# Kernel tuning notes

Measured on AMD Instinct MI355X. Metric: run time of the kernel, lower is better.

## Reference

```python
import jax, jax.numpy as jnp
import numpy as np

B, T, C = 4, 2048, 1024
H = 16
D = C // H  # head_dim = 64


def setup_inputs() -> dict:
    key = jax.random.key(0)
    ks = jax.random.split(key, 9)
    s = 1.0 / np.sqrt(C)
    return {
        "x": jax.random.normal(ks[0], (B, T, C), dtype=jnp.float32),
        "Wq": jax.random.normal(ks[1], (C, C), dtype=jnp.float32) * s,
        "bq": jnp.zeros((C,), dtype=jnp.float32),
        "Wk": jax.random.normal(ks[2], (C, C), dtype=jnp.float32) * s,
        "bk": jnp.zeros((C,), dtype=jnp.float32),
        "Wv": jax.random.normal(ks[3], (C, C), dtype=jnp.float32) * s,
        "bv": jnp.zeros((C,), dtype=jnp.float32),
        "Wp": jax.random.normal(ks[4], (C, C), dtype=jnp.float32) * s,
        "bp": jnp.zeros((C,), dtype=jnp.float32),
    }


def reference(x, Wq, bq, Wk, bk, Wv, bv, Wp, bp):
    # Linear projections; reshape to [B, H, T, D]
    def split_heads(y):
        return y.reshape(B, T, H, D).transpose(0, 2, 1, 3)

    q = split_heads(x @ Wq + bq)
    k = split_heads(x @ Wk + bk)
    v = split_heads(x @ Wv + bv)

    scale = 1.0 / np.sqrt(D)
    att = jnp.einsum('bhqd,bhkd->bhqk', q, k) * scale  # [B,H,T,T]
    att = jax.nn.softmax(att, axis=-1)
    # dropout with p=0.0 is identity
    out = jnp.einsum('bhqk,bhkd->bhqd', att, v)        # [B,H,T,D]
    out = out.transpose(0, 2, 1, 3).reshape(B, T, C)
    return out @ Wp + bp
```

## Files before the change

### kernel.cpp

```cpp
#include <hip/hip_runtime.h>


#define B_ 4
#define T_ 2048
#define C_ 1024
#define H_ 16
#define D_ 64

typedef float  f32x4  __attribute__((ext_vector_type(4)));
typedef __bf16 bf16x8 __attribute__((ext_vector_type(8)));
typedef __bf16 bf16x4 __attribute__((ext_vector_type(4)));
typedef __bf16 bf16x2 __attribute__((ext_vector_type(2)));
typedef unsigned uint2v __attribute__((ext_vector_type(2)));

typedef const __attribute__((address_space(1))) void gv_t;
typedef __attribute__((address_space(3))) void lds_t;

__device__ __forceinline__ void async_load16(const void* g, void* l) {
  __builtin_amdgcn_global_load_lds((gv_t*)g, (lds_t*)l, 16, 0, 0);
}

__device__ __forceinline__ float fast_exp2(float x) {
#if __has_builtin(__builtin_amdgcn_exp2f)
  return __builtin_amdgcn_exp2f(x);
#else
  return exp2f(x);
#endif
}

__device__ __forceinline__ void pl16_swap(unsigned& a, unsigned& b) {
#if __has_builtin(__builtin_amdgcn_permlane16_swap)
  uint2v r = __builtin_amdgcn_permlane16_swap(a, b, false, false);
  a = r[0];
  b = r[1];
#else
  asm("v_permlane16_swap_b32 %0, %1" : "+v"(a), "+v"(b));
#endif
}

__global__ __launch_bounds__(256) void cast_f32_bf16(
    const float* __restrict__ in, __bf16* __restrict__ out, int n) {
  int i = (blockIdx.x * 256 + threadIdx.x) * 8;
  if (i >= n) return;
  float4 a = *(const float4*)(in + i);
  float4 b = *(const float4*)(in + i + 4);
  bf16x8 o;
  o[0] = (__bf16)a.x; o[1] = (__bf16)a.y; o[2] = (__bf16)a.z; o[3] = (__bf16)a.w;
  o[4] = (__bf16)b.x; o[5] = (__bf16)b.y; o[6] = (__bf16)b.z; o[7] = (__bf16)b.w;
  *(bf16x8*)(out + i) = o;
}

__global__ __launch_bounds__(256) void transpose_cast_w(
    const float* __restrict__ W0, const float* __restrict__ W1,
    const float* __restrict__ W2, const float* __restrict__ W3,
    __bf16* __restrict__ out) {
  int z = blockIdx.z;
  const float* W = (z == 0) ? W0 : (z == 1) ? W1 : (z == 2) ? W2 : W3;
  __bf16* o = out + (size_t)z * (C_ * C_);
  __shared__ __align__(16) __bf16 sT[64][72];
  int tid = threadIdx.x;
  int n0 = blockIdx.x * 64, k0 = blockIdx.y * 64;
#pragma unroll
  for (int i = 0; i < 4; i++) {
    int s = tid + i * 256;
    int kr = s >> 4, nc = (s & 15) * 4;
    float4 v = *(const float4*)&W[(size_t)(k0 + kr) * C_ + n0 + nc];
    bf16x4 t;
    t[0] = (__bf16)v.x; t[1] = (__bf16)v.y; t[2] = (__bf16)v.z; t[3] = (__bf16)v.w;
    *(bf16x4*)&sT[kr][nc] = t;
  }
  __syncthreads();
#pragma unroll
  for (int i = 0; i < 2; i++) {
    int s = tid + i * 256;
    int nr = s >> 3, kc = (s & 7) * 8;
    bf16x8 ov;
#pragma unroll
    for (int j = 0; j < 8; j++) ov[j] = sT[kc + j][nr];
    *(bf16x8*)&o[(size_t)(n0 + nr) * C_ + k0 + kc] = ov;
  }
}

template <typename OutT, int EPI>
__device__ __forceinline__ void gemm_body(
    const __bf16* __restrict__ A, const __bf16* __restrict__ Bt,
    const float* __restrict__ bias, OutT* __restrict__ C, int M, int N, int K) {
  __shared__ __align__(16) __bf16 sA[128 * 32];
  __shared__ __align__(16) __bf16 sB[128 * 32];
  int tid = threadIdx.x, lane = tid & 63, wave = tid >> 6;
  int lr = lane & 15, quad = lane >> 4;
  int m0 = blockIdx.y * 128, n0 = blockIdx.x * 128;
  int wm = (wave & 1) * 64, wn = (wave >> 1) * 64;

  const f32x4 zero = {0.f, 0.f, 0.f, 0.f};
  f32x4 acc[4][4];
#pragma unroll
  for (int i = 0; i < 4; i++)
#pragma unroll
    for (int j = 0; j < 4; j++) acc[i][j] = zero;

  for (int k0 = 0; k0 < K; k0 += 32) {
    __syncthreads();
#pragma unroll
    for (int i = 0; i < 2; i++) {
      int s = tid + i * 256;
      int r = s >> 2, c8 = (s & 3) * 8;
      async_load16(A + (size_t)(m0 + r) * K + k0 + c8, &sA[s * 8]);
      async_load16(Bt + (size_t)(n0 + r) * K + k0 + c8, &sB[s * 8]);
    }
    __syncthreads();
    bf16x8 af[4], bfr[4];
#pragma unroll
    for (int mt = 0; mt < 4; mt++)
      af[mt] = *(const bf16x8*)&sA[(wm + mt * 16 + lr) * 32 + quad * 8];
#pragma unroll
    for (int nt = 0; nt < 4; nt++)
      bfr[nt] = *(const bf16x8*)&sB[(wn + nt * 16 + lr) * 32 + quad * 8];
#pragma unroll
    for (int mt = 0; mt < 4; mt++)
#pragma unroll
      for (int nt = 0; nt < 4; nt++)
        acc[mt][nt] = __builtin_amdgcn_mfma_f32_16x16x32_bf16(
            af[mt], bfr[nt], acc[mt][nt], 0, 0, 0);
  }
  if (EPI == 0) {
#pragma unroll
    for (int mt = 0; mt < 4; mt++) {
#pragma unroll
      for (int nt = 0; nt < 4; nt++) {
        int n = n0 + wn + nt * 16 + lr;
        float bv = bias[n];
#pragma unroll
        for (int r = 0; r < 4; r++) {
          int m = m0 + wm + mt * 16 + quad * 4 + r;
          C[(size_t)m * N + n] = (OutT)(acc[mt][nt][r] + bv);
        }
      }
    }
  } else {
    int bb = m0 >> 11;
    int mloc0 = (m0 & (T_ - 1)) + wm;
    __bf16* Ct = (__bf16*)C;
#pragma unroll
    for (int mt = 0; mt < 4; mt++) {
      int pos = ((quad & 1) << 5) | ((((quad >> 1) << 1) | (mt & 1)) << 3) |
                ((mt >> 1) << 2);
#pragma unroll
      for (int nt = 0; nt < 4; nt++) {
        int n = n0 + wn + nt * 16 + lr;
        float bv = bias[n];
        bf16x4 ov;
#pragma unroll
        for (int r = 0; r < 4; r++) ov[r] = (__bf16)(acc[mt][nt][r] + bv);
        *(bf16x4*)&Ct[((size_t)bb * C_ + n) * T_ + mloc0 + pos] = ov;
      }
    }
  }
}

__global__ __launch_bounds__(256) void gemm_qkv_kernel(
    const __bf16* __restrict__ A, const __bf16* __restrict__ WT,
    const float* __restrict__ b0, const float* __restrict__ b1,
    const float* __restrict__ b2, __bf16* __restrict__ qkbase,
    __bf16* __restrict__ Vt) {
  int z = blockIdx.z;
  if (z == 2) {
    gemm_body<__bf16, 1>(A, WT + (size_t)2 * C_ * C_, b2, Vt, B_ * T_, C_, C_);
  } else {
    const float* bias = (z == 0) ? b0 : b1;
    gemm_body<__bf16, 0>(A, WT + (size_t)z * C_ * C_, bias,
                         qkbase + (size_t)z * (B_ * T_) * C_, B_ * T_, C_, C_);
  }
}

__global__ __launch_bounds__(256) void gemm_proj_kernel(
    const __bf16* __restrict__ A, const __bf16* __restrict__ Bt,
    const float* __restrict__ bias, float* __restrict__ C) {
  gemm_body<float, 0>(A, Bt, bias, C, B_ * T_, C_, C_);
}

__global__ __launch_bounds__(256) void attn_kernel(
    const __bf16* __restrict__ Q, const __bf16* __restrict__ K,
    const __bf16* __restrict__ Vt, __bf16* __restrict__ O) {
  __shared__ __align__(16) __bf16 sK[64 * 72];
  __shared__ __align__(16) __bf16 sV[64 * 72];
  int tid = threadIdx.x, wave = tid >> 6, lane = tid & 63;
  int lr = lane & 15, quad = lane >> 4;
  int bh = blockIdx.y;
  int b = bh >> 4, h = bh & 15;
  int qw = blockIdx.x * 128 + wave * 32;

  bf16x8 aq[2][2];
#pragma unroll
  for (int s = 0; s < 2; s++) {
    const __bf16* qp =
        Q + ((size_t)(b * T_ + qw + s * 16 + lr)) * C_ + h * D_ + quad * 8;
    aq[s][0] = *(const bf16x8*)qp;
    aq[s][1] = *(const bf16x8*)(qp + 32);
  }

  bf16x8 onesf;
#pragma unroll
  for (int j = 0; j < 8; j++) onesf[j] = (__bf16)1.0f;

  const f32x4 zero = {0.f, 0.f, 0.f, 0.f};
  f32x4 accO[2][4];
  f32x4 accL[2] = {zero, zero};
#pragma unroll
  for (int s = 0; s < 2; s++)
#pragma unroll
    for (int d = 0; d < 4; d++) accO[s][d] = zero;

  const float cexp = 0.125f * 1.44269504088896340736f;

  int srow[2], sc8[2];
#pragma unroll
  for (int i = 0; i < 2; i++) {
    int s = tid + i * 256;
    srow[i] = s >> 3;
    sc8[i] = (s & 7) * 8;
  }

  bf16x8 kreg[2], vreg[2];
#pragma unroll
  for (int i = 0; i < 2; i++) {
    kreg[i] = *(const bf16x8*)(K + ((size_t)(b * T_ + srow[i])) * C_ + h * D_ + sc8[i]);
    vreg[i] = *(const bf16x8*)(Vt + ((size_t)(bh * D_ + srow[i])) * T_ + sc8[i]);
  }

  for (int k0 = 0; k0 < T_; k0 += 64) {
    __syncthreads();
#pragma unroll
    for (int i = 0; i < 2; i++) {
      *(bf16x8*)&sK[srow[i] * 72 + sc8[i]] = kreg[i];
      *(bf16x8*)&sV[srow[i] * 72 + sc8[i]] = vreg[i];
    }
    __syncthreads();

    if (k0 + 64 < T_) {
      int kn = k0 + 64;
#pragma unroll
      for (int i = 0; i < 2; i++) {
        kreg[i] = *(const bf16x8*)(K + ((size_t)(b * T_ + kn + srow[i])) * C_ + h * D_ + sc8[i]);
        vreg[i] = *(const bf16x8*)(Vt + ((size_t)(bh * D_ + srow[i])) * T_ + kn + sc8[i]);
      }
    }

    unsigned pw[2][4][2];
#pragma unroll
    for (int nt = 0; nt < 4; nt++) {
      bf16x8 bk0 = *(const bf16x8*)&sK[(nt * 16 + lr) * 72 + quad * 8];
      bf16x8 bk1 = *(const bf16x8*)&sK[(nt * 16 + lr) * 72 + 32 + quad * 8];
#pragma unroll
      for (int s = 0; s < 2; s++) {
        f32x4 z = zero;
        z = __builtin_amdgcn_mfma_f32_16x16x32_bf16(bk0, aq[s][0], z, 0, 0, 0);
        z = __builtin_amdgcn_mfma_f32_16x16x32_bf16(bk1, aq[s][1], z, 0, 0, 0);
        union { bf16x2 h; unsigned u; } t0, t1;
        t0.h[0] = (__bf16)fast_exp2(z[0] * cexp);
        t0.h[1] = (__bf16)fast_exp2(z[1] * cexp);
        t1.h[0] = (__bf16)fast_exp2(z[2] * cexp);
        t1.h[1] = (__bf16)fast_exp2(z[3] * cexp);
        pw[s][nt][0] = t0.u;
        pw[s][nt][1] = t1.u;
      }
    }

    bf16x8 bpA[2], bpB[2];
#pragma unroll
    for (int s = 0; s < 2; s++) {
      unsigned a0 = pw[s][0][0], b0 = pw[s][1][0]; pl16_swap(a0, b0);
      unsigned a1 = pw[s][0][1], b1 = pw[s][1][1]; pl16_swap(a1, b1);
      unsigned a2 = pw[s][2][0], b2 = pw[s][3][0]; pl16_swap(a2, b2);
      unsigned a3 = pw[s][2][1], b3 = pw[s][3][1]; pl16_swap(a3, b3);
      union { unsigned u[4]; bf16x8 v; } pA, pB;
      pA.u[0] = a0; pA.u[1] = a1; pA.u[2] = a2; pA.u[3] = a3;
      pB.u[0] = b0; pB.u[1] = b1; pB.u[2] = b2; pB.u[3] = b3;
      bpA[s] = pA.v;
      bpB[s] = pB.v;
      accL[s] = __builtin_amdgcn_mfma_f32_16x16x32_bf16(onesf, bpA[s], accL[s], 0, 0, 0);
      accL[s] = __builtin_amdgcn_mfma_f32_16x16x32_bf16(onesf, bpB[s], accL[s], 0, 0, 0);
    }
#pragma unroll
    for (int dt = 0; dt < 4; dt++) {
      bf16x8 av0 = *(const bf16x8*)&sV[(dt * 16 + lr) * 72 + quad * 8];
      bf16x8 av1 = *(const bf16x8*)&sV[(dt * 16 + lr) * 72 + 32 + quad * 8];
#pragma unroll
      for (int s = 0; s < 2; s++) {
        accO[s][dt] = __builtin_amdgcn_mfma_f32_16x16x32_bf16(av0, bpA[s], accO[s][dt], 0, 0, 0);
        accO[s][dt] = __builtin_amdgcn_mfma_f32_16x16x32_bf16(av1, bpB[s], accO[s][dt], 0, 0, 0);
      }
    }
  }

#pragma unroll
  for (int s = 0; s < 2; s++) {
    float inv = 1.0f / accL[s][0];
    __bf16* op =
        O + ((size_t)(b * T_ + qw + s * 16 + lr)) * C_ + h * D_ + quad * 4;
#pragma unroll
    for (int dt = 0; dt < 4; dt++) {
      bf16x4 ov;
#pragma unroll
      for (int r = 0; r < 4; r++) ov[r] = (__bf16)(accO[s][dt][r] * inv);
      *(bf16x4*)&op[dt * 16] = ov;
    }
  }
}

extern "C" void kernel_launch(void* const* d_in, const int* in_sizes, int n_in,
                              void* d_out, int out_size, void* d_ws, size_t ws_size,
                              hipStream_t stream) {
  const float* x  = (const float*)d_in[0];
  const float* Wq = (const float*)d_in[1];
  const float* bq = (const float*)d_in[2];
  const float* Wk = (const float*)d_in[3];
  const float* bk = (const float*)d_in[4];
  const float* Wv = (const float*)d_in[5];
  const float* bv = (const float*)d_in[6];
  const float* Wp = (const float*)d_in[7];
  const float* bp = (const float*)d_in[8];
  float* out = (float*)d_out;

  char* ws = (char*)d_ws;
  const size_t MB = 1024 * 1024;
  __bf16* xb    = (__bf16*)(ws + 0 * MB);
  __bf16* WT    = (__bf16*)(ws + 16 * MB);
  __bf16* Qb    = (__bf16*)(ws + 24 * MB);
  __bf16* Kb    = Qb + (size_t)(B_ * T_) * C_;
  __bf16* Vt    = Kb + (size_t)(B_ * T_) * C_;
  __bf16* attnb = (__bf16*)(ws + 72 * MB);
  __bf16* WpT   = WT + (size_t)3 * C_ * C_;

  cast_f32_bf16<<<dim3(4096), dim3(256), 0, stream>>>(x, xb, B_ * T_ * C_);
  transpose_cast_w<<<dim3(16, 16, 4), dim3(256), 0, stream>>>(Wq, Wk, Wv, Wp, WT);
  gemm_qkv_kernel<<<dim3(8, 64, 3), dim3(256), 0, stream>>>(xb, WT, bq, bk, bv, Qb, Vt);
  attn_kernel<<<dim3(16, 64), dim3(256), 0, stream>>>(Qb, Kb, Vt, attnb);
  gemm_proj_kernel<<<dim3(8, 64), dim3(256), 0, stream>>>(attnb, WpT, bp, out);
}
```

Baseline: 291.1 us.

## Double query rows per attention wave and fold softmax scale into Q projection

The attention kernel now handles 64 query rows per wave (256 per block) instead of 32, so each K/V tile loaded into LDS and each K fragment read from LDS is reused across twice as many queries. This halves the grid to 512 blocks. Separately, the softmax scale times log2(e) is applied in the Q projection epilogue, which removes a multiply per score before exp2. The trade-offs are higher register pressure from the larger accumulators, fewer blocks for occupancy, and Q now rounded to bf16 after scaling.

Measured after the change: 279.3 us. 4.1% less time.

```diff
diff --git a/kernel.cpp b/kernel.cpp
--- a/kernel.cpp
+++ b/kernel.cpp
@@ -6,6 +6,8 @@
 #define C_ 1024
 #define H_ 16
 #define D_ 64
+
+#define QSCALE 0.18033688011112042f
 
 typedef float  f32x4  __attribute__((ext_vector_type(4)));
 typedef __bf16 bf16x8 __attribute__((ext_vector_type(8)));
@@ -84,7 +86,8 @@
 template <typename OutT, int EPI>
 __device__ __forceinline__ void gemm_body(
     const __bf16* __restrict__ A, const __bf16* __restrict__ Bt,
-    const float* __restrict__ bias, OutT* __restrict__ C, int M, int N, int K) {
+    const float* __restrict__ bias, OutT* __restrict__ C, int M, int N, int K,
+    float scale) {
   __shared__ __align__(16) __bf16 sA[128 * 32];
   __shared__ __align__(16) __bf16 sB[128 * 32];
   int tid = threadIdx.x, lane = tid & 63, wave = tid >> 6;
@@ -133,7 +136,7 @@
 #pragma unroll
         for (int r = 0; r < 4; r++) {
           int m = m0 + wm + mt * 16 + quad * 4 + r;
-          C[(size_t)m * N + n] = (OutT)(acc[mt][nt][r] + bv);
+          C[(size_t)m * N + n] = (OutT)((acc[mt][nt][r] + bv) * scale);
         }
       }
     }
@@ -165,18 +168,21 @@
     __bf16* __restrict__ Vt) {
   int z = blockIdx.z;
   if (z == 2) {
-    gemm_body<__bf16, 1>(A, WT + (size_t)2 * C_ * C_, b2, Vt, B_ * T_, C_, C_);
+    gemm_body<__bf16, 1>(A, WT + (size_t)2 * C_ * C_, b2, Vt, B_ * T_, C_, C_,
+                         1.0f);
   } else {
     const float* bias = (z == 0) ? b0 : b1;
+    float scale = (z == 0) ? QSCALE : 1.0f;
     gemm_body<__bf16, 0>(A, WT + (size_t)z * C_ * C_, bias,
-                         qkbase + (size_t)z * (B_ * T_) * C_, B_ * T_, C_, C_);
+                         qkbase + (size_t)z * (B_ * T_) * C_, B_ * T_, C_, C_,
+                         scale);
   }
 }
 
 __global__ __launch_bounds__(256) void gemm_proj_kernel(
     const __bf16* __restrict__ A, const __bf16* __restrict__ Bt,
     const float* __restrict__ bias, float* __restrict__ C) {
-  gemm_body<float, 0>(A, Bt, bias, C, B_ * T_, C_, C_);
+  gemm_body<float, 0>(A, Bt, bias, C, B_ * T_, C_, C_, 1.0f);
 }
 
 __global__ __launch_bounds__(256) void attn_kernel(
@@ -188,11 +194,11 @@
   int lr = lane & 15, quad = lane >> 4;
   int bh = blockIdx.y;
   int b = bh >> 4, h = bh & 15;
-  int qw = blockIdx.x * 128 + wave * 32;
-
-  bf16x8 aq[2][2];
-#pragma unroll
-  for (int s = 0; s < 2; s++) {
+  int qw = blockIdx.x * 256 + wave * 64;
+
+  bf16x8 aq[4][2];
+#pragma unroll
+  for (int s = 0; s < 4; s++) {
     const __bf16* qp =
         Q + ((size_t)(b * T_ + qw + s * 16 + lr)) * C_ + h * D_ + quad * 8;
     aq[s][0] = *(const bf16x8*)qp;
@@ -204,14 +210,12 @@
   for (int j = 0; j < 8; j++) onesf[j] = (__bf16)1.0f;
 
   const f32x4 zero = {0.f, 0.f, 0.f, 0.f};
-  f32x4 accO[2][4];
-  f32x4 accL[2] = {zero, zero};
-#pragma unroll
-  for (int s = 0; s < 2; s++)
+  f32x4 accO[4][4];
+  f32x4 accL[4] = {zero, zero, zero, zero};
+#pragma unroll
+  for (int s = 0; s < 4; s++)
 #pragma unroll
     for (int d = 0; d < 4; d++) accO[s][d] = zero;
-
-  const float cexp = 0.125f * 1.44269504088896340736f;
 
   int srow[2], sc8[2];
 #pragma unroll
@@ -246,33 +250,34 @@
       }
     }
 
-    unsigned pw[2][4][2];
+    bf16x8 bkf[4][2];
 #pragma unroll
     for (int nt = 0; nt < 4; nt++) {
-      bf16x8 bk0 = *(const bf16x8*)&sK[(nt * 16 + lr) * 72 + quad * 8];
-      bf16x8 bk1 = *(const bf16x8*)&sK[(nt * 16 + lr) * 72 + 32 + quad * 8];
-#pragma unroll
-      for (int s = 0; s < 2; s++) {
+      bkf[nt][0] = *(const bf16x8*)&sK[(nt * 16 + lr) * 72 + quad * 8];
+      bkf[nt][1] = *(const bf16x8*)&sK[(nt * 16 + lr) * 72 + 32 + quad * 8];
+    }
+
+    bf16x8 bpA[4], bpB[4];
+#pragma unroll
+    for (int s = 0; s < 4; s++) {
+      unsigned pw[4][2];
+#pragma unroll
+      for (int nt = 0; nt < 4; nt++) {
         f32x4 z = zero;
-        z = __builtin_amdgcn_mfma_f32_16x16x32_bf16(bk0, aq[s][0], z, 0, 0, 0);
-        z = __builtin_amdgcn_mfma_f32_16x16x32_bf16(bk1, aq[s][1], z, 0, 0, 0);
+        z = __builtin_amdgcn_mfma_f32_16x16x32_bf16(bkf[nt][0], aq[s][0], z, 0, 0, 0);
+        z = __builtin_amdgcn_mfma_f32_16x16x32_bf16(bkf[nt][1], aq[s][1], z, 0, 0, 0);
         union { bf16x2 h; unsigned u; } t0, t1;
-        t0.h[0] = (__bf16)fast_exp2(z[0] * cexp);
-        t0.h[1] = (__bf16)fast_exp2(z[1] * cexp);
-        t1.h[0] = (__bf16)fast_exp2(z[2] * cexp);
-        t1.h[1] = (__bf16)fast_exp2(z[3] * cexp);
-        pw[s][nt][0] = t0.u;
-        pw[s][nt][1] = t1.u;
-      }
-    }
-
-    bf16x8 bpA[2], bpB[2];
-#pragma unroll
-    for (int s = 0; s < 2; s++) {
-      unsigned a0 = pw[s][0][0], b0 = pw[s][1][0]; pl16_swap(a0, b0);
-      unsigned a1 = pw[s][0][1], b1 = pw[s][1][1]; pl16_swap(a1, b1);
-      unsigned a2 = pw[s][2][0], b2 = pw[s][3][0]; pl16_swap(a2, b2);
-      unsigned a3 = pw[s][2][1], b3 = pw[s][3][1]; pl16_swap(a3, b3);
+        t0.h[0] = (__bf16)fast_exp2(z[0]);
+        t0.h[1] = (__bf16)fast_exp2(z[1]);
+        t1.h[0] = (__bf16)fast_exp2(z[2]);
+        t1.h[1] = (__bf16)fast_exp2(z[3]);
+        pw[nt][0] = t0.u;
+        pw[nt][1] = t1.u;
+      }
+      unsigned a0 = pw[0][0], b0 = pw[1][0]; pl16_swap(a0, b0);
+      unsigned a1 = pw[0][1], b1 = pw[1][1]; pl16_swap(a1, b1);
+      unsigned a2 = pw[2][0], b2 = pw[3][0]; pl16_swap(a2, b2);
+      unsigned a3 = pw[2][1], b3 = pw[3][1]; pl16_swap(a3, b3);
       union { unsigned u[4]; bf16x8 v; } pA, pB;
       pA.u[0] = a0; pA.u[1] = a1; pA.u[2] = a2; pA.u[3] = a3;
       pB.u[0] = b0; pB.u[1] = b1; pB.u[2] = b2; pB.u[3] = b3;
@@ -286,7 +291,7 @@
       bf16x8 av0 = *(const bf16x8*)&sV[(dt * 16 + lr) * 72 + quad * 8];
       bf16x8 av1 = *(const bf16x8*)&sV[(dt * 16 + lr) * 72 + 32 + quad * 8];
 #pragma unroll
-      for (int s = 0; s < 2; s++) {
+      for (int s = 0; s < 4; s++) {
         accO[s][dt] = __builtin_amdgcn_mfma_f32_16x16x32_bf16(av0, bpA[s], accO[s][dt], 0, 0, 0);
         accO[s][dt] = __builtin_amdgcn_mfma_f32_16x16x32_bf16(av1, bpB[s], accO[s][dt], 0, 0, 0);
       }
@@ -294,7 +299,7 @@
   }
 
 #pragma unroll
-  for (int s = 0; s < 2; s++) {
+  for (int s = 0; s < 4; s++) {
     float inv = 1.0f / accL[s][0];
     __bf16* op =
         O + ((size_t)(b * T_ + qw + s * 16 + lr)) * C_ + h * D_ + quad * 4;
@@ -335,6 +340,6 @@
   cast_f32_bf16<<<dim3(4096), dim3(256), 0, stream>>>(x, xb, B_ * T_ * C_);
   transpose_cast_w<<<dim3(16, 16, 4), dim3(256), 0, stream>>>(Wq, Wk, Wv, Wp, WT);
   gemm_qkv_kernel<<<dim3(8, 64, 3), dim3(256), 0, stream>>>(xb, WT, bq, bk, bv, Qb, Vt);
-  attn_kernel<<<dim3(16, 64), dim3(256), 0, stream>>>(Qb, Kb, Vt, attnb);
+  attn_kernel<<<dim3(8, 64), dim3(256), 0, stream>>>(Qb, Kb, Vt, attnb);
   gemm_proj_kernel<<<dim3(8, 64), dim3(256), 0, stream>>>(attnb, WpT, bp, out);
 }
```
